# Performance work log

Measured on AMD Instinct MI355X. Metric: run time of the kernel, lower is better.

The kernel has to match this reference:

```python
import jax, jax.numpy as jnp
import numpy as np

N_NODES = 50000
N_EDGES = 800000
D = 128
RRELU_SLOPE = (1.0 / 8.0 + 1.0 / 3.0) / 2.0  # eval-mode RReLU = leaky relu with mean slope 11/48


def setup_inputs() -> dict:
    key = jax.random.key(0)
    ks = jax.random.split(key, 10)
    s = 1.0 / np.sqrt(D)
    return {
        "node_feats": jax.random.normal(ks[0], (N_NODES, D), dtype=jnp.float32),
        "edge_feats": jax.random.normal(ks[1], (N_EDGES, D), dtype=jnp.float32),
        "src": jax.random.randint(ks[2], (N_EDGES,), 0, N_NODES, dtype=jnp.int32),
        "dst": jax.random.randint(ks[3], (N_EDGES,), 0, N_NODES, dtype=jnp.int32),
        "Wn0": jax.random.uniform(ks[4], (D, D), jnp.float32, -s, s),
        "Ws0": jax.random.uniform(ks[5], (D, D), jnp.float32, -s, s),
        "Wi0": jax.random.uniform(ks[6], (D, D), jnp.float32, -s, s),
        "Wn1": jax.random.uniform(ks[7], (D, D), jnp.float32, -s, s),
        "Ws1": jax.random.uniform(ks[8], (D, D), jnp.float32, -s, s),
        "Wi1": jax.random.uniform(ks[9], (D, D), jnp.float32, -s, s),
    }


def _layer(h, edge_feats, src, dst, deg, iso, Wn, Ws, Wi, num_nodes):
    # per-edge message: neigh_linear(src_h + edge_h)
    msg = (h[src] + edge_feats) @ Wn.T  # [E, H]
    # mean aggregate to destination; nodes with no in-edges get 0 (DGL semantics)
    agg = jax.ops.segment_sum(msg, dst, num_segments=num_nodes)
    agg = agg / jnp.maximum(deg, 1.0)[:, None]
    # self-loop message, replaced by isolated-node message where in_degree == 0
    self_msg = jnp.where(iso[:, None], h @ Wi.T, h @ Ws.T)
    x = agg + self_msg
    # RReLU in eval mode = leaky relu with slope (lower+upper)/2
    return jnp.where(x >= 0, x, RRELU_SLOPE * x)


def reference(node_feats, edge_feats, src, dst, Wn0, Ws0, Wi0, Wn1, Ws1, Wi1):
    num_nodes = node_feats.shape[0]
    deg = jax.ops.segment_sum(
        jnp.ones(src.shape[0], dtype=node_feats.dtype), dst, num_segments=num_nodes
    )
    iso = deg == 0
    h = _layer(node_feats, edge_feats, src, dst, deg, iso, Wn0, Ws0, Wi0, num_nodes)
    h = _layer(h, edge_feats, src, dst, deg, iso, Wn1, Ws1, Wi1, num_nodes)
    return h
```

## Files before the change

kernel.cpp:

```cpp
#include <hip/hip_runtime.h>
#include <hip/hip_bf16.h>

#define N_NODES 50000
#define N_EDGES 800000
#define D 128
#define D2 64

static constexpr float SLOPE = 11.0f / 48.0f;

typedef __attribute__((ext_vector_type(8))) short bf16x8;
typedef __attribute__((ext_vector_type(4))) float f32x4;

__device__ __forceinline__ float bf_lo(unsigned int v) { return __uint_as_float(v << 16); }
__device__ __forceinline__ float bf_hi(unsigned int v) { return __uint_as_float(v & 0xffff0000u); }

__device__ __forceinline__ unsigned short f2bf(float x) {
    __hip_bfloat16 b = __float2bfloat16(x);
    return *(unsigned short*)&b;
}

__device__ __forceinline__ unsigned int pack_bf2(float lo, float hi) {
    return ((unsigned int)f2bf(hi) << 16) | (unsigned int)f2bf(lo);
}

__device__ __forceinline__ bf16x8 cvt8(const float* __restrict__ p) {
    f32x4 lo = *(const f32x4*)p;
    f32x4 hi = *(const f32x4*)(p + 4);
    bf16x8 r;
#pragma unroll
    for (int i = 0; i < 4; ++i) r[i] = (short)f2bf(lo[i]);
#pragma unroll
    for (int i = 0; i < 4; ++i) r[4 + i] = (short)f2bf(hi[i]);
    return r;
}


__global__ void k_count(const int* __restrict__ dst, int* __restrict__ deg) {
    int e = blockIdx.x * 256 + threadIdx.x;
    if (e < N_EDGES) atomicAdd(&deg[dst[e]], 1);
}

__global__ void k_scan1(const int* __restrict__ deg, int* __restrict__ offs,
                        int* __restrict__ part) {
    __shared__ int sm[256];
    int t = threadIdx.x;
    int i = blockIdx.x * 256 + t;
    int v = (i < N_NODES) ? deg[i] : 0;
    int orig = v;
    sm[t] = v;
    __syncthreads();
    for (int off = 1; off < 256; off <<= 1) {
        int x = (t >= off) ? sm[t - off] : 0;
        __syncthreads();
        sm[t] += x;
        __syncthreads();
    }
    if (i < N_NODES) offs[i] = sm[t] - orig;
    if (t == 255) part[blockIdx.x] = sm[t];
}

__global__ void k_scan2(int* __restrict__ part, int nb) {
    __shared__ int sm[256];
    int t = threadIdx.x;
    int v = (t < nb) ? part[t] : 0;
    int orig = v;
    sm[t] = v;
    __syncthreads();
    for (int off = 1; off < 256; off <<= 1) {
        int x = (t >= off) ? sm[t - off] : 0;
        __syncthreads();
        sm[t] += x;
        __syncthreads();
    }
    if (t < nb) part[t] = sm[t] - orig;
}

__global__ void k_scan3(int* __restrict__ offs, const int* __restrict__ part) {
    int i = blockIdx.x * 256 + threadIdx.x;
    if (i < N_NODES) offs[i] += part[blockIdx.x];
}

__global__ void k_fill(const int* __restrict__ src, const int* __restrict__ dst,
                       const int* __restrict__ offs, int* __restrict__ cur,
                       int2* __restrict__ csr) {
    int e = blockIdx.x * 256 + threadIdx.x;
    if (e < N_EDGES) {
        int d = dst[e];
        int p = offs[d] + atomicAdd(&cur[d], 1);
        csr[p] = make_int2(src[e], e);
    }
}


__global__ void k_agg_ef(const float2* __restrict__ h,
                         const float2* __restrict__ ef,
                         const int2* __restrict__ csr,
                         const int* __restrict__ offs, const int* __restrict__ deg,
                         unsigned int* __restrict__ efsum,
                         unsigned int* __restrict__ pre) {
    int node = blockIdx.x * 4 + (threadIdx.x >> 6);
    if (node >= N_NODES) return;
    int lane = threadIdx.x & 63;
    int start = offs[node];
    int cnt = deg[node];
    float hx = 0.f, hy = 0.f, ex = 0.f, ey = 0.f;
    for (int k = 0; k < cnt; ++k) {
        int2 se = csr[start + k];
        float2 hv = h[(size_t)se.x * D2 + lane];
        float2 ev = ef[(size_t)se.y * D2 + lane];
        hx += hv.x;
        hy += hv.y;
        ex += ev.x;
        ey += ev.y;
    }
    efsum[(size_t)node * D2 + lane] = pack_bf2(ex, ey);
    float inv = 1.0f / fmaxf((float)cnt, 1.0f);
    pre[(size_t)node * D2 + lane] = pack_bf2((hx + ex) * inv, (hy + ey) * inv);
}


__global__ void k_agg2(const unsigned int* __restrict__ h,
                       const int2* __restrict__ csr,
                       const int* __restrict__ offs, const int* __restrict__ deg,
                       const unsigned int* __restrict__ efsum,
                       unsigned int* __restrict__ pre) {
    int node = blockIdx.x * 4 + (threadIdx.x >> 6);
    if (node >= N_NODES) return;
    int lane = threadIdx.x & 63;
    int start = offs[node];
    int cnt = deg[node];
    unsigned int es = efsum[(size_t)node * D2 + lane];
    float ax = bf_lo(es), ay = bf_hi(es);
    for (int k = 0; k < cnt; ++k) {
        int2 se = csr[start + k];
        unsigned int v = h[(size_t)se.x * D2 + lane];
        ax += bf_lo(v);
        ay += bf_hi(v);
    }
    float inv = 1.0f / fmaxf((float)cnt, 1.0f);
    pre[(size_t)node * D2 + lane] = pack_bf2(ax * inv, ay * inv);
}


template <int A2_F32, int OUT_F32>
__global__ void k_gemm(const unsigned short* __restrict__ A1,
                       const void* __restrict__ A2v,
                       const float* __restrict__ W1,
                       const float* __restrict__ W2,
                       void* __restrict__ outv) {
    int wave = threadIdx.x >> 6;
    int lane = threadIdx.x & 63;
    int quad = lane >> 4;
    int r16 = lane & 15;
    int m0 = (blockIdx.x * 4 + wave) * 32;

    f32x4 acc[2][8];
#pragma unroll
    for (int mt = 0; mt < 2; ++mt)
#pragma unroll
        for (int nt = 0; nt < 8; ++nt) acc[mt][nt] = (f32x4){0.f, 0.f, 0.f, 0.f};

    int rowA0 = min(m0 + r16, N_NODES - 1);
    int rowA1 = min(m0 + 16 + r16, N_NODES - 1);

#pragma unroll
    for (int ks = 0; ks < 8; ++ks) {
        int koff = (ks & 3) * 32 + quad * 8;
        bf16x8 a0, a1;
        if (ks < 4) {
            a0 = *(const bf16x8*)(A1 + (size_t)rowA0 * D + koff);
            a1 = *(const bf16x8*)(A1 + (size_t)rowA1 * D + koff);
        } else if (A2_F32) {
            const float* A2 = (const float*)A2v;
            a0 = cvt8(A2 + (size_t)rowA0 * D + koff);
            a1 = cvt8(A2 + (size_t)rowA1 * D + koff);
        } else {
            const unsigned short* A2 = (const unsigned short*)A2v;
            a0 = *(const bf16x8*)(A2 + (size_t)rowA0 * D + koff);
            a1 = *(const bf16x8*)(A2 + (size_t)rowA1 * D + koff);
        }
        const float* Wsrc = (ks < 4) ? W1 : W2;
#pragma unroll
        for (int nt = 0; nt < 8; ++nt) {
            bf16x8 b = cvt8(Wsrc + (size_t)(nt * 16 + r16) * D + koff);
            acc[0][nt] = __builtin_amdgcn_mfma_f32_16x16x32_bf16(a0, b, acc[0][nt], 0, 0, 0);
            acc[1][nt] = __builtin_amdgcn_mfma_f32_16x16x32_bf16(a1, b, acc[1][nt], 0, 0, 0);
        }
    }

#pragma unroll
    for (int mt = 0; mt < 2; ++mt) {
#pragma unroll
        for (int r = 0; r < 4; ++r) {
            int row = m0 + mt * 16 + quad * 4 + r;
            if (row < N_NODES) {
#pragma unroll
                for (int nt = 0; nt < 8; ++nt) {
                    float x = acc[mt][nt][r];
                    x = (x >= 0.f) ? x : x * SLOPE;
                    if (OUT_F32)
                        ((float*)outv)[(size_t)row * D + nt * 16 + r16] = x;
                    else
                        ((unsigned short*)outv)[(size_t)row * D + nt * 16 + r16] = f2bf(x);
                }
            }
        }
    }
}


__global__ void k_fixup1(const float* __restrict__ h,
                         const float* __restrict__ Wi,
                         const int* __restrict__ deg,
                         unsigned short* __restrict__ out) {
    int node = blockIdx.x * 4 + (threadIdx.x >> 6);
    if (node >= N_NODES) return;
    if (deg[node] != 0) return;
    int lane = threadIdx.x & 63;
    float a0 = 0.f, a1 = 0.f;
    const float* hrow = h + (size_t)node * D;
    for (int k = 0; k < D; ++k) {
        float hk = hrow[k];
        a0 += hk * Wi[(size_t)lane * D + k];
        a1 += hk * Wi[(size_t)(lane + 64) * D + k];
    }
    a0 = (a0 >= 0.f) ? a0 : a0 * SLOPE;
    a1 = (a1 >= 0.f) ? a1 : a1 * SLOPE;
    out[(size_t)node * D + lane] = f2bf(a0);
    out[(size_t)node * D + lane + 64] = f2bf(a1);
}

__global__ void k_fixup2(const unsigned short* __restrict__ h,
                         const float* __restrict__ Wi,
                         const int* __restrict__ deg,
                         float* __restrict__ out) {
    int node = blockIdx.x * 4 + (threadIdx.x >> 6);
    if (node >= N_NODES) return;
    if (deg[node] != 0) return;
    int lane = threadIdx.x & 63;
    float a0 = 0.f, a1 = 0.f;
    const unsigned short* hrow = h + (size_t)node * D;
    for (int k = 0; k < D; ++k) {
        float hk = __uint_as_float(((unsigned int)hrow[k]) << 16);
        a0 += hk * Wi[(size_t)lane * D + k];
        a1 += hk * Wi[(size_t)(lane + 64) * D + k];
    }
    a0 = (a0 >= 0.f) ? a0 : a0 * SLOPE;
    a1 = (a1 >= 0.f) ? a1 : a1 * SLOPE;
    out[(size_t)node * D + lane] = a0;
    out[(size_t)node * D + lane + 64] = a1;
}


extern "C" void kernel_launch(void* const* d_in, const int* in_sizes, int n_in,
                              void* d_out, int out_size, void* d_ws, size_t ws_size,
                              hipStream_t stream) {
    const float* node_feats = (const float*)d_in[0];
    const float* edge_feats = (const float*)d_in[1];
    const int* src = (const int*)d_in[2];
    const int* dst = (const int*)d_in[3];
    const float* Wn0 = (const float*)d_in[4];
    const float* Ws0 = (const float*)d_in[5];
    const float* Wi0 = (const float*)d_in[6];
    const float* Wn1 = (const float*)d_in[7];
    const float* Ws1 = (const float*)d_in[8];
    const float* Wi1 = (const float*)d_in[9];

    char* ws = (char*)d_ws;
    size_t o = 0;
    auto alloc = [&](size_t bytes) -> char* {
        char* p = ws + o;
        o += (bytes + 255) & ~size_t(255);
        return p;
    };
    int* deg = (int*)alloc((size_t)N_NODES * 4);
    int* cur = (int*)alloc((size_t)N_NODES * 4);
    int* offs = (int*)alloc((size_t)N_NODES * 4);
    int* part = (int*)alloc(1024);
    int2* csr = (int2*)alloc((size_t)N_EDGES * 8);
    unsigned int* efsum = (unsigned int*)alloc((size_t)N_NODES * D * 2);
    unsigned int* pre = (unsigned int*)alloc((size_t)N_NODES * D * 2);
    unsigned int* h1 = (unsigned int*)alloc((size_t)N_NODES * D * 2);

    hipMemsetAsync(deg, 0, 2 * (((size_t)N_NODES * 4 + 255) & ~size_t(255)), stream);

    int ebl = (N_EDGES + 255) / 256;
    int nbl = (N_NODES + 255) / 256;
    int nwb = (N_NODES + 3) / 4;
    int gbl = (N_NODES + 127) / 128;

    k_count<<<ebl, 256, 0, stream>>>(dst, deg);
    k_scan1<<<nbl, 256, 0, stream>>>(deg, offs, part);
    k_scan2<<<1, 256, 0, stream>>>(part, nbl);
    k_scan3<<<nbl, 256, 0, stream>>>(offs, part);
    k_fill<<<ebl, 256, 0, stream>>>(src, dst, offs, cur, csr);

    k_agg_ef<<<nwb, 256, 0, stream>>>((const float2*)node_feats,
                                      (const float2*)edge_feats,
                                      csr, offs, deg, efsum, pre);
    k_gemm<1, 0><<<gbl, 256, 0, stream>>>((const unsigned short*)pre, (const void*)node_feats,
                                          Wn0, Ws0, (void*)h1);
    k_fixup1<<<nwb, 256, 0, stream>>>(node_feats, Wi0, deg, (unsigned short*)h1);

    k_agg2<<<nwb, 256, 0, stream>>>(h1, csr, offs, deg, efsum, pre);
    k_gemm<0, 1><<<gbl, 256, 0, stream>>>((const unsigned short*)pre, (const void*)h1,
                                          Wn1, Ws1, d_out);
    k_fixup2<<<nwb, 256, 0, stream>>>((const unsigned short*)h1, Wi1, deg, (float*)d_out);
}
```

Before: 873.1 us.

## Pre-convert features and weights to bf16, widen gather loads, compact isolated-node fixups

Adds kernels that convert node features and the four GEMM weight matrices to bf16 once up front, so the GEMMs and the first aggregation read bf16 instead of converting fp32 on every load. The aggregation kernels now split edges across half-waves or quarter-waves with wider vector loads and combine partial sums with shuffles, aiming for more memory-level parallelism per node. The isolated-node fixups use a compacted list built by an atomic kernel and launch a small fixed grid instead of one wave per node. The trade is extra conversion passes and launches, and layer-1 features are rounded to bf16 before both the gather and the self/isolated terms.

```diff
diff --git a/kernel.cpp b/kernel.cpp
--- a/kernel.cpp
+++ b/kernel.cpp
@@ -10,6 +10,8 @@
 
 typedef __attribute__((ext_vector_type(8))) short bf16x8;
 typedef __attribute__((ext_vector_type(4))) float f32x4;
+typedef __attribute__((ext_vector_type(2))) unsigned int u32x2;
+typedef __attribute__((ext_vector_type(4))) unsigned int u32x4;
 
 __device__ __forceinline__ float bf_lo(unsigned int v) { return __uint_as_float(v << 16); }
 __device__ __forceinline__ float bf_hi(unsigned int v) { return __uint_as_float(v & 0xffff0000u); }
@@ -23,15 +25,35 @@
     return ((unsigned int)f2bf(hi) << 16) | (unsigned int)f2bf(lo);
 }
 
-__device__ __forceinline__ bf16x8 cvt8(const float* __restrict__ p) {
-    f32x4 lo = *(const f32x4*)p;
-    f32x4 hi = *(const f32x4*)(p + 4);
-    bf16x8 r;
-#pragma unroll
-    for (int i = 0; i < 4; ++i) r[i] = (short)f2bf(lo[i]);
-#pragma unroll
-    for (int i = 0; i < 4; ++i) r[4 + i] = (short)f2bf(hi[i]);
-    return r;
+
+__global__ void k_cvt_nf(const f32x4* __restrict__ in, u32x4* __restrict__ out) {
+    int i = blockIdx.x * 256 + threadIdx.x;
+    if (i >= N_NODES * D / 8) return;
+    f32x4 lo = in[2 * i];
+    f32x4 hi = in[2 * i + 1];
+    u32x4 o;
+    o.x = pack_bf2(lo[0], lo[1]);
+    o.y = pack_bf2(lo[2], lo[3]);
+    o.z = pack_bf2(hi[0], hi[1]);
+    o.w = pack_bf2(hi[2], hi[3]);
+    out[i] = o;
+}
+
+__global__ void k_cvt_w(const float* __restrict__ Wn0, const float* __restrict__ Ws0,
+                        const float* __restrict__ Wn1, const float* __restrict__ Ws1,
+                        unsigned int* __restrict__ out) {
+    int i = blockIdx.x * 256 + threadIdx.x;
+    int m = i >> 11;
+    int j = i & 2047;
+    const float* W = (m == 0) ? Wn0 : (m == 1) ? Ws0 : (m == 2) ? Wn1 : Ws1;
+    f32x4 lo = ((const f32x4*)W)[2 * j];
+    f32x4 hi = ((const f32x4*)W)[2 * j + 1];
+    u32x4 o;
+    o.x = pack_bf2(lo[0], lo[1]);
+    o.y = pack_bf2(lo[2], lo[3]);
+    o.z = pack_bf2(hi[0], hi[1]);
+    o.w = pack_bf2(hi[2], hi[3]);
+    *(u32x4*)(out + (size_t)m * 8192 + 4 * j) = o;
 }
 
 
@@ -91,9 +113,18 @@
     }
 }
 
-
-__global__ void k_agg_ef(const float2* __restrict__ h,
-                         const float2* __restrict__ ef,
+__global__ void k_iso(const int* __restrict__ deg, int* __restrict__ isolist,
+                      int* __restrict__ niso) {
+    int i = blockIdx.x * 256 + threadIdx.x;
+    if (i < N_NODES && deg[i] == 0) {
+        int p = atomicAdd(niso, 1);
+        isolist[p] = i;
+    }
+}
+
+
+__global__ void k_agg_ef(const unsigned int* __restrict__ nfb,
+                         const f32x4* __restrict__ ef,
                          const int2* __restrict__ csr,
                          const int* __restrict__ offs, const int* __restrict__ deg,
                          unsigned int* __restrict__ efsum,
@@ -101,21 +132,43 @@
     int node = blockIdx.x * 4 + (threadIdx.x >> 6);
     if (node >= N_NODES) return;
     int lane = threadIdx.x & 63;
+    int half = lane >> 5;
+    int c = lane & 31;
     int start = offs[node];
     int cnt = deg[node];
-    float hx = 0.f, hy = 0.f, ex = 0.f, ey = 0.f;
-    for (int k = 0; k < cnt; ++k) {
+    f32x4 ae = {0.f, 0.f, 0.f, 0.f};
+    f32x4 ah = {0.f, 0.f, 0.f, 0.f};
+#pragma unroll 2
+    for (int k = half; k < cnt; k += 2) {
         int2 se = csr[start + k];
-        float2 hv = h[(size_t)se.x * D2 + lane];
-        float2 ev = ef[(size_t)se.y * D2 + lane];
-        hx += hv.x;
-        hy += hv.y;
-        ex += ev.x;
-        ey += ev.y;
-    }
-    efsum[(size_t)node * D2 + lane] = pack_bf2(ex, ey);
+        f32x4 ev = ef[(size_t)se.y * 32 + c];
+        u32x2 hv = *(const u32x2*)(nfb + (size_t)se.x * D2 + 2 * c);
+        ae[0] += ev[0];
+        ae[1] += ev[1];
+        ae[2] += ev[2];
+        ae[3] += ev[3];
+        ah[0] += bf_lo(hv.x);
+        ah[1] += bf_hi(hv.x);
+        ah[2] += bf_lo(hv.y);
+        ah[3] += bf_hi(hv.y);
+    }
+#pragma unroll
+    for (int i = 0; i < 4; ++i) {
+        ae[i] += __shfl_xor(ae[i], 32);
+        ah[i] += __shfl_xor(ah[i], 32);
+    }
     float inv = 1.0f / fmaxf((float)cnt, 1.0f);
-    pre[(size_t)node * D2 + lane] = pack_bf2((hx + ex) * inv, (hy + ey) * inv);
+    if (half == 0) {
+        u32x2 eo;
+        eo.x = pack_bf2(ae[0], ae[1]);
+        eo.y = pack_bf2(ae[2], ae[3]);
+        *(u32x2*)(efsum + (size_t)node * D2 + 2 * c) = eo;
+    } else {
+        u32x2 po;
+        po.x = pack_bf2((ah[0] + ae[0]) * inv, (ah[1] + ae[1]) * inv);
+        po.y = pack_bf2((ah[2] + ae[2]) * inv, (ah[3] + ae[3]) * inv);
+        *(u32x2*)(pre + (size_t)node * D2 + 2 * c) = po;
+    }
 }
 
 
@@ -127,26 +180,55 @@
     int node = blockIdx.x * 4 + (threadIdx.x >> 6);
     if (node >= N_NODES) return;
     int lane = threadIdx.x & 63;
+    int q = lane >> 4;
+    int g = lane & 15;
     int start = offs[node];
     int cnt = deg[node];
-    unsigned int es = efsum[(size_t)node * D2 + lane];
-    float ax = bf_lo(es), ay = bf_hi(es);
-    for (int k = 0; k < cnt; ++k) {
+    float a[8] = {0.f, 0.f, 0.f, 0.f, 0.f, 0.f, 0.f, 0.f};
+#pragma unroll 2
+    for (int k = q; k < cnt; k += 4) {
         int2 se = csr[start + k];
-        unsigned int v = h[(size_t)se.x * D2 + lane];
-        ax += bf_lo(v);
-        ay += bf_hi(v);
-    }
-    float inv = 1.0f / fmaxf((float)cnt, 1.0f);
-    pre[(size_t)node * D2 + lane] = pack_bf2(ax * inv, ay * inv);
-}
-
-
-template <int A2_F32, int OUT_F32>
+        u32x4 hv = *(const u32x4*)(h + (size_t)se.x * D2 + 4 * g);
+        a[0] += bf_lo(hv.x);
+        a[1] += bf_hi(hv.x);
+        a[2] += bf_lo(hv.y);
+        a[3] += bf_hi(hv.y);
+        a[4] += bf_lo(hv.z);
+        a[5] += bf_hi(hv.z);
+        a[6] += bf_lo(hv.w);
+        a[7] += bf_hi(hv.w);
+    }
+#pragma unroll
+    for (int i = 0; i < 8; ++i) {
+        a[i] += __shfl_xor(a[i], 16);
+        a[i] += __shfl_xor(a[i], 32);
+    }
+    if (q == 0) {
+        u32x4 es = *(const u32x4*)(efsum + (size_t)node * D2 + 4 * g);
+        float inv = 1.0f / fmaxf((float)cnt, 1.0f);
+        float r0 = (a[0] + bf_lo(es.x)) * inv;
+        float r1 = (a[1] + bf_hi(es.x)) * inv;
+        float r2 = (a[2] + bf_lo(es.y)) * inv;
+        float r3 = (a[3] + bf_hi(es.y)) * inv;
+        float r4 = (a[4] + bf_lo(es.z)) * inv;
+        float r5 = (a[5] + bf_hi(es.z)) * inv;
+        float r6 = (a[6] + bf_lo(es.w)) * inv;
+        float r7 = (a[7] + bf_hi(es.w)) * inv;
+        u32x4 o;
+        o.x = pack_bf2(r0, r1);
+        o.y = pack_bf2(r2, r3);
+        o.z = pack_bf2(r4, r5);
+        o.w = pack_bf2(r6, r7);
+        *(u32x4*)(pre + (size_t)node * D2 + 4 * g) = o;
+    }
+}
+
+
+template <int OUT_F32>
 __global__ void k_gemm(const unsigned short* __restrict__ A1,
-                       const void* __restrict__ A2v,
-                       const float* __restrict__ W1,
-                       const float* __restrict__ W2,
+                       const unsigned short* __restrict__ A2,
+                       const unsigned short* __restrict__ W1,
+                       const unsigned short* __restrict__ W2,
                        void* __restrict__ outv) {
     int wave = threadIdx.x >> 6;
     int lane = threadIdx.x & 63;
@@ -166,23 +248,13 @@
 #pragma unroll
     for (int ks = 0; ks < 8; ++ks) {
         int koff = (ks & 3) * 32 + quad * 8;
-        bf16x8 a0, a1;
-        if (ks < 4) {
-            a0 = *(const bf16x8*)(A1 + (size_t)rowA0 * D + koff);
-            a1 = *(const bf16x8*)(A1 + (size_t)rowA1 * D + koff);
-        } else if (A2_F32) {
-            const float* A2 = (const float*)A2v;
-            a0 = cvt8(A2 + (size_t)rowA0 * D + koff);
-            a1 = cvt8(A2 + (size_t)rowA1 * D + koff);
-        } else {
-            const unsigned short* A2 = (const unsigned short*)A2v;
-            a0 = *(const bf16x8*)(A2 + (size_t)rowA0 * D + koff);
-            a1 = *(const bf16x8*)(A2 + (size_t)rowA1 * D + koff);
-        }
-        const float* Wsrc = (ks < 4) ? W1 : W2;
+        const unsigned short* Asrc = (ks < 4) ? A1 : A2;
+        bf16x8 a0 = *(const bf16x8*)(Asrc + (size_t)rowA0 * D + koff);
+        bf16x8 a1 = *(const bf16x8*)(Asrc + (size_t)rowA1 * D + koff);
+        const unsigned short* Wsrc = (ks < 4) ? W1 : W2;
 #pragma unroll
         for (int nt = 0; nt < 8; ++nt) {
-            bf16x8 b = cvt8(Wsrc + (size_t)(nt * 16 + r16) * D + koff);
+            bf16x8 b = *(const bf16x8*)(Wsrc + (size_t)(nt * 16 + r16) * D + koff);
             acc[0][nt] = __builtin_amdgcn_mfma_f32_16x16x32_bf16(a0, b, acc[0][nt], 0, 0, 0);
             acc[1][nt] = __builtin_amdgcn_mfma_f32_16x16x32_bf16(a1, b, acc[1][nt], 0, 0, 0);
         }
@@ -209,46 +281,52 @@
 }
 
 
-__global__ void k_fixup1(const float* __restrict__ h,
+__global__ void k_fixup1(const unsigned int* __restrict__ nfb,
                          const float* __restrict__ Wi,
-                         const int* __restrict__ deg,
+                         const int* __restrict__ isolist, const int* __restrict__ niso,
                          unsigned short* __restrict__ out) {
-    int node = blockIdx.x * 4 + (threadIdx.x >> 6);
-    if (node >= N_NODES) return;
-    if (deg[node] != 0) return;
-    int lane = threadIdx.x & 63;
-    float a0 = 0.f, a1 = 0.f;
-    const float* hrow = h + (size_t)node * D;
-    for (int k = 0; k < D; ++k) {
-        float hk = hrow[k];
-        a0 += hk * Wi[(size_t)lane * D + k];
-        a1 += hk * Wi[(size_t)(lane + 64) * D + k];
-    }
-    a0 = (a0 >= 0.f) ? a0 : a0 * SLOPE;
-    a1 = (a1 >= 0.f) ? a1 : a1 * SLOPE;
-    out[(size_t)node * D + lane] = f2bf(a0);
-    out[(size_t)node * D + lane + 64] = f2bf(a1);
+    int w = blockIdx.x * 4 + (threadIdx.x >> 6);
+    int lane = threadIdx.x & 63;
+    int n = *niso;
+    for (int t = w; t < n; t += gridDim.x * 4) {
+        int node = isolist[t];
+        const unsigned int* hrow = nfb + (size_t)node * D2;
+        float a0 = 0.f, a1 = 0.f;
+        for (int ku = 0; ku < D2; ++ku) {
+            unsigned int v = hrow[ku];
+            float h0 = bf_lo(v), h1 = bf_hi(v);
+            a0 += h0 * Wi[(size_t)lane * D + 2 * ku] + h1 * Wi[(size_t)lane * D + 2 * ku + 1];
+            a1 += h0 * Wi[(size_t)(lane + 64) * D + 2 * ku] +
+                  h1 * Wi[(size_t)(lane + 64) * D + 2 * ku + 1];
+        }
+        a0 = (a0 >= 0.f) ? a0 : a0 * SLOPE;
+        a1 = (a1 >= 0.f) ? a1 : a1 * SLOPE;
+        out[(size_t)node * D + lane] = f2bf(a0);
+        out[(size_t)node * D + lane + 64] = f2bf(a1);
+    }
 }
 
 __global__ void k_fixup2(const unsigned short* __restrict__ h,
                          const float* __restrict__ Wi,
-                         const int* __restrict__ deg,
+                         const int* __restrict__ isolist, const int* __restrict__ niso,
                          float* __restrict__ out) {
-    int node = blockIdx.x * 4 + (threadIdx.x >> 6);
-    if (node >= N_NODES) return;
-    if (deg[node] != 0) return;
-    int lane = threadIdx.x & 63;
-    float a0 = 0.f, a1 = 0.f;
-    const unsigned short* hrow = h + (size_t)node * D;
-    for (int k = 0; k < D; ++k) {
-        float hk = __uint_as_float(((unsigned int)hrow[k]) << 16);
-        a0 += hk * Wi[(size_t)lane * D + k];
-        a1 += hk * Wi[(size_t)(lane + 64) * D + k];
-    }
-    a0 = (a0 >= 0.f) ? a0 : a0 * SLOPE;
-    a1 = (a1 >= 0.f) ? a1 : a1 * SLOPE;
-    out[(size_t)node * D + lane] = a0;
-    out[(size_t)node * D + lane + 64] = a1;
+    int w = blockIdx.x * 4 + (threadIdx.x >> 6);
+    int lane = threadIdx.x & 63;
+    int n = *niso;
+    for (int t = w; t < n; t += gridDim.x * 4) {
+        int node = isolist[t];
+        const unsigned short* hrow = h + (size_t)node * D;
+        float a0 = 0.f, a1 = 0.f;
+        for (int k = 0; k < D; ++k) {
+            float hk = __uint_as_float(((unsigned int)hrow[k]) << 16);
+            a0 += hk * Wi[(size_t)lane * D + k];
+            a1 += hk * Wi[(size_t)(lane + 64) * D + k];
+        }
+        a0 = (a0 >= 0.f) ? a0 : a0 * SLOPE;
+        a1 = (a1 >= 0.f) ? a1 : a1 * SLOPE;
+        out[(size_t)node * D + lane] = a0;
+        out[(size_t)node * D + lane + 64] = a1;
+    }
 }
 
 
@@ -275,35 +353,46 @@
     };
     int* deg = (int*)alloc((size_t)N_NODES * 4);
     int* cur = (int*)alloc((size_t)N_NODES * 4);
+    int* niso = (int*)alloc(256);
     int* offs = (int*)alloc((size_t)N_NODES * 4);
     int* part = (int*)alloc(1024);
+    int* isolist = (int*)alloc((size_t)N_NODES * 4);
     int2* csr = (int2*)alloc((size_t)N_EDGES * 8);
     unsigned int* efsum = (unsigned int*)alloc((size_t)N_NODES * D * 2);
     unsigned int* pre = (unsigned int*)alloc((size_t)N_NODES * D * 2);
     unsigned int* h1 = (unsigned int*)alloc((size_t)N_NODES * D * 2);
-
-    hipMemsetAsync(deg, 0, 2 * (((size_t)N_NODES * 4 + 255) & ~size_t(255)), stream);
+    unsigned int* nfb = (unsigned int*)alloc((size_t)N_NODES * D * 2);
+    unsigned int* wbf = (unsigned int*)alloc(4 * 8192 * 4);
+
+    hipMemsetAsync(deg, 0, 2 * (((size_t)N_NODES * 4 + 255) & ~size_t(255)) + 256, stream);
 
     int ebl = (N_EDGES + 255) / 256;
     int nbl = (N_NODES + 255) / 256;
     int nwb = (N_NODES + 3) / 4;
     int gbl = (N_NODES + 127) / 128;
 
+    k_cvt_nf<<<(N_NODES * D / 8 + 255) / 256, 256, 0, stream>>>((const f32x4*)node_feats,
+                                                                (u32x4*)nfb);
+    k_cvt_w<<<32, 256, 0, stream>>>(Wn0, Ws0, Wn1, Ws1, wbf);
     k_count<<<ebl, 256, 0, stream>>>(dst, deg);
     k_scan1<<<nbl, 256, 0, stream>>>(deg, offs, part);
     k_scan2<<<1, 256, 0, stream>>>(part, nbl);
     k_scan3<<<nbl, 256, 0, stream>>>(offs, part);
     k_fill<<<ebl, 256, 0, stream>>>(src, dst, offs, cur, csr);
-
-    k_agg_ef<<<nwb, 256, 0, stream>>>((const float2*)node_feats,
-                                      (const float2*)edge_feats,
-                                      csr, offs, deg, efsum, pre);
-    k_gemm<1, 0><<<gbl, 256, 0, stream>>>((const unsigned short*)pre, (const void*)node_feats,
-                                          Wn0, Ws0, (void*)h1);
-    k_fixup1<<<nwb, 256, 0, stream>>>(node_feats, Wi0, deg, (unsigned short*)h1);
+    k_iso<<<nbl, 256, 0, stream>>>(deg, isolist, niso);
+
+    const unsigned short* Wn0b = (const unsigned short*)(wbf + 0 * 8192);
+    const unsigned short* Ws0b = (const unsigned short*)(wbf + 1 * 8192);
+    const unsigned short* Wn1b = (const unsigned short*)(wbf + 2 * 8192);
+    const unsigned short* Ws1b = (const unsigned short*)(wbf + 3 * 8192);
+
+    k_agg_ef<<<nwb, 256, 0, stream>>>(nfb, (const f32x4*)edge_feats, csr, offs, deg, efsum, pre);
+    k_gemm<0><<<gbl, 256, 0, stream>>>((const unsigned short*)pre, (const unsigned short*)nfb,
+                                       Wn0b, Ws0b, (void*)h1);
+    k_fixup1<<<32, 256, 0, stream>>>(nfb, Wi0, isolist, niso, (unsigned short*)h1);
 
     k_agg2<<<nwb, 256, 0, stream>>>(h1, csr, offs, deg, efsum, pre);
-    k_gemm<0, 1><<<gbl, 256, 0, stream>>>((const unsigned short*)pre, (const void*)h1,
-                                          Wn1, Ws1, d_out);
-    k_fixup2<<<nwb, 256, 0, stream>>>((const unsigned short*)h1, Wi1, deg, (float*)d_out);
-}
+    k_gemm<1><<<gbl, 256, 0, stream>>>((const unsigned short*)pre, (const unsigned short*)h1,
+                                       Wn1b, Ws1b, d_out);
+    k_fixup2<<<32, 256, 0, stream>>>((const unsigned short*)h1, Wi1, isolist, niso, (float*)d_out);
+}
```

Measured after the change: 757.0 us. 13.3% less time.
